# Kernel tuning notes

Measured on AMD Instinct MI355X. Metric: run time of the kernel, lower is better.

Reference implementation:

```python
import jax, jax.numpy as jnp
import numpy as np

VOCAB = 32000
EMBED = 512
DEP_SIZE = 64
QKV = 512
B, S = 16, 1024
NEG = -1e10


def setup_inputs() -> dict:
    key = jax.random.key(0)
    ks = jax.random.split(key, 16)
    inputs = jax.random.randint(ks[0], (B, S), 0, VOCAB)
    dependency = jax.random.randint(ks[1], (B, S, S), 0, DEP_SIZE)
    embed_table = jax.random.normal(ks[2], (VOCAB, EMBED), dtype=jnp.float32) * 0.02
    dep_table = jax.random.normal(ks[3], (DEP_SIZE, 1), dtype=jnp.float32) * 0.02
    dep_table = dep_table.at[0].set(0.0)  # padding_idx=0
    sc = 1.0 / np.sqrt(EMBED)
    Wq = jax.random.normal(ks[4], (EMBED, QKV), dtype=jnp.float32) * sc
    bq = jnp.zeros((QKV,), jnp.float32)
    Wk = jax.random.normal(ks[5], (EMBED, QKV), dtype=jnp.float32) * sc
    bk = jnp.zeros((QKV,), jnp.float32)
    Wv = jax.random.normal(ks[6], (EMBED, QKV), dtype=jnp.float32) * sc
    bv = jnp.zeros((QKV,), jnp.float32)
    scv = 1.0 / np.sqrt(QKV)
    W1 = jax.random.normal(ks[7], (QKV, QKV), dtype=jnp.float32) * scv
    b1 = jnp.zeros((QKV,), jnp.float32)
    W2 = jax.random.normal(ks[8], (QKV, QKV), dtype=jnp.float32) * scv
    b2 = jnp.zeros((QKV,), jnp.float32)
    return dict(inputs=inputs, dependency=dependency, embed_table=embed_table,
                dep_table=dep_table, Wq=Wq, bq=bq, Wk=Wk, bk=bk, Wv=Wv, bv=bv,
                W1=W1, b1=b1, W2=W2, b2=b2)


def reference(inputs, dependency, embed_table, dep_table, Wq, bq, Wk, bk, Wv, bv, W1, b1, W2, b2):
    x = jnp.take(embed_table, inputs, axis=0)                  # [B,S,E]
    dep_emb = jnp.take(dep_table, dependency, axis=0)[..., 0]  # [B,S,S]
    q = x @ Wq + bq                                            # [B,S,D]
    k = x @ Wk + bk
    v = x @ Wv + bv
    attn = jnp.einsum('bqd,bkd->bqk', q, k) * dep_emb          # [B,S,S]
    attn = jnp.where(dependency == 0, NEG, attn)
    weights = jax.nn.softmax(attn, axis=-1)
    wm = jnp.einsum('bqk,bkd->bqd', weights, v)                # fused weighted sum
    wm = jnp.tanh(wm @ W1 + b1) @ W2 + b2
    return wm, weights
```

## Files before the change

kernel.cpp:

```cpp
#include <hip/hip_runtime.h>

typedef __attribute__((ext_vector_type(8))) short short8;
typedef __attribute__((ext_vector_type(4))) float floatx4;

__device__ __forceinline__ unsigned short f2b(float f) {
  unsigned int u = __float_as_uint(f);
  unsigned int r = (u + 0x7FFFu + ((u >> 16) & 1u)) >> 16;
  return (unsigned short)r;
}
__device__ __forceinline__ uint4 ld8f(const float* p) {
  float4 a = *(const float4*)p;
  float4 b = *(const float4*)(p + 4);
  uint4 r;
  r.x = (unsigned int)f2b(a.x) | ((unsigned int)f2b(a.y) << 16);
  r.y = (unsigned int)f2b(a.z) | ((unsigned int)f2b(a.w) << 16);
  r.z = (unsigned int)f2b(b.x) | ((unsigned int)f2b(b.y) << 16);
  r.w = (unsigned int)f2b(b.z) | ((unsigned int)f2b(b.w) << 16);
  return r;
}

#define GLL(g, l) __builtin_amdgcn_global_load_lds( \
    (const __attribute__((address_space(1))) unsigned int*)(g), \
    (__attribute__((address_space(3))) unsigned int*)(l), 16, 0, 0)

__device__ __forceinline__ void xcd_swz(int& bx, int& by, int& bz) {
  const int nx = gridDim.x, ny = gridDim.y;
  const int nwg = nx * ny * gridDim.z;
  const int lbid = blockIdx.x + nx * (blockIdx.y + ny * blockIdx.z);
  const int s = (lbid & 7) * (nwg >> 3) + (lbid >> 3);
  bx = s % nx; by = (s / nx) % ny; bz = s / (nx * ny);
}

__device__ __forceinline__ void kloop(const unsigned short* __restrict__ A,
                                      const unsigned short* __restrict__ B,
                                      int K, unsigned short* ldsA, unsigned short* ldsB,
                                      floatx4 (&acc)[2][4])
{
  const int tid = threadIdx.x;
  const int w = tid >> 6, lane = tid & 63;
  const int quad = lane >> 4, l16 = lane & 15;
  const int wy = w >> 1, wx = w & 1;
  const int rsa = 16 * w + (lane >> 2);
  const int rsb = 32 * w + (lane >> 2);
  const int ks = (lane & 3) * 8;
  const int loa  = w * 512 + lane * 8;
  const int lob0 = w * 1024 + lane * 8;
  const int lob1 = lob0 + 512;
  const unsigned short* a0 = A + (size_t)rsa * K + ks;
  const unsigned short* b0 = B + (size_t)rsb * K + ks;
  const unsigned short* b1 = b0 + (size_t)16 * K;

  for (int k0 = 0; k0 < K; k0 += 32) {
    __syncthreads();
    GLL(a0 + k0, &ldsA[loa]);
    GLL(b0 + k0, &ldsB[lob0]);
    GLL(b1 + k0, &ldsB[lob1]);
    __syncthreads();
    short8 af[2], bf[4];
#pragma unroll
    for (int i = 0; i < 2; i++)
      af[i] = *(const short8*)&ldsA[(wy * 32 + i * 16 + l16) * 32 + quad * 8];
#pragma unroll
    for (int j = 0; j < 4; j++)
      bf[j] = *(const short8*)&ldsB[(wx * 64 + j * 16 + l16) * 32 + quad * 8];
#pragma unroll
    for (int i = 0; i < 2; i++)
#pragma unroll
      for (int j = 0; j < 4; j++)
        acc[i][j] = __builtin_amdgcn_mfma_f32_16x16x32_bf16(af[i], bf[j], acc[i][j], 0, 0, 0);
  }
}

__global__ __launch_bounds__(256, 4) void gemm_qkv(
    const unsigned short* __restrict__ x,
    const unsigned short* __restrict__ WT,
    const float* __restrict__ bq, const float* __restrict__ bk, const float* __restrict__ bv,
    unsigned short* __restrict__ q, unsigned short* __restrict__ kx, unsigned short* __restrict__ v)
{
  __shared__ unsigned short ldsA[2048], ldsB[4096];
  int bx, by, bz;
  xcd_swz(bx, by, bz);
  const int m0 = by * 64, n0 = bx * 128;
  floatx4 acc[2][4];
#pragma unroll
  for (int i = 0; i < 2; i++)
#pragma unroll
    for (int j = 0; j < 4; j++) acc[i][j] = (floatx4){0.f, 0.f, 0.f, 0.f};

  kloop(x + (size_t)m0 * 512, WT + (size_t)n0 * 512, 512, ldsA, ldsB, acc);

  const int seg = n0 >> 9, nloc = n0 & 511;
  unsigned short* C = seg == 0 ? q : (seg == 1 ? kx : v);
  const float* bias = seg == 0 ? bq : (seg == 1 ? bk : bv);
  const int lane = threadIdx.x & 63, w = threadIdx.x >> 6;
  const int quad = lane >> 4, l16 = lane & 15, wy = w >> 1, wx = w & 1;
  float bvv[4];
#pragma unroll
  for (int j = 0; j < 4; j++) bvv[j] = bias[nloc + wx * 64 + j * 16 + l16];
#pragma unroll
  for (int i = 0; i < 2; i++)
#pragma unroll
    for (int r = 0; r < 4; r++) {
      int m = m0 + wy * 32 + i * 16 + quad * 4 + r;
      unsigned short* crow = C + (size_t)m * 512 + nloc + wx * 64 + l16;
#pragma unroll
      for (int j = 0; j < 4; j++) crow[j * 16] = f2b(acc[i][j][r] + bvv[j]);
    }
}

template<int CF32, int ACT>
__global__ __launch_bounds__(256, 4) void gemm2(
    const unsigned short* __restrict__ A, const unsigned short* __restrict__ Bt,
    const float* __restrict__ bias, void* __restrict__ Cv,
    int N, int K, long aB, long bB, long cB)
{
  __shared__ unsigned short ldsA[2048], ldsB[4096];
  int bx, by, bz;
  xcd_swz(bx, by, bz);
  const int b = bz;
  const int m0 = by * 64, n0 = bx * 128;
  floatx4 acc[2][4];
#pragma unroll
  for (int i = 0; i < 2; i++)
#pragma unroll
    for (int j = 0; j < 4; j++) acc[i][j] = (floatx4){0.f, 0.f, 0.f, 0.f};

  kloop(A + (size_t)b * aB + (size_t)m0 * K, Bt + (size_t)b * bB + (size_t)n0 * K,
        K, ldsA, ldsB, acc);

  const int lane = threadIdx.x & 63, w = threadIdx.x >> 6;
  const int quad = lane >> 4, l16 = lane & 15, wy = w >> 1, wx = w & 1;
  float bvv[4];
#pragma unroll
  for (int j = 0; j < 4; j++)
    bvv[j] = bias ? bias[n0 + wx * 64 + j * 16 + l16] : 0.f;
  float*          Cf = (float*)Cv          + (size_t)b * cB;
  unsigned short* Ch = (unsigned short*)Cv + (size_t)b * cB;
#pragma unroll
  for (int i = 0; i < 2; i++)
#pragma unroll
    for (int r = 0; r < 4; r++) {
      int m = m0 + wy * 32 + i * 16 + quad * 4 + r;
      size_t base = (size_t)m * N + n0 + wx * 64 + l16;
#pragma unroll
      for (int j = 0; j < 4; j++) {
        float vv = acc[i][j][r] + bvv[j];
        if (ACT == 1) vv = tanhf(vv);
        if (CF32) Cf[base + j * 16] = vv;
        else      Ch[base + j * 16] = f2b(vv);
      }
    }
}

#define CST 132
__global__ __launch_bounds__(256, 4) void score_kernel(
    const unsigned short* __restrict__ Q, const unsigned short* __restrict__ Km,
    const int* __restrict__ dep, const float* __restrict__ dept,
    float* __restrict__ E)
{
  __shared__ union {
    struct { unsigned short a[2048]; unsigned short b[4096]; } s;
    float c[32 * CST];
  } sm;
  __shared__ float dtab[64];
  const int tid = threadIdx.x;
  if (tid < 64) dtab[tid] = dept[tid];

  int bx, by, bz;
  xcd_swz(bx, by, bz);
  const int b = bz;
  const int m0 = by * 64, n0 = bx * 128;
  floatx4 acc[2][4];
#pragma unroll
  for (int i = 0; i < 2; i++)
#pragma unroll
    for (int j = 0; j < 4; j++) acc[i][j] = (floatx4){0.f, 0.f, 0.f, 0.f};

  kloop(Q + (size_t)b * (1024 * 512) + (size_t)m0 * 512,
        Km + (size_t)b * (1024 * 512) + (size_t)n0 * 512,
        512, sm.s.a, sm.s.b, acc);

  const int lane = tid & 63, w = tid >> 6;
  const int quad = lane >> 4, l16 = lane & 15, wy = w >> 1, wx = w & 1;
  const int* depb = dep + (size_t)b * 1024 * 1024;
  float* Eb = E + (size_t)b * 1024 * 1024;
  const int cr = tid >> 3, cb = (tid & 7) * 16;

#pragma unroll
  for (int i = 0; i < 2; i++) {
    __syncthreads();
#pragma unroll
    for (int j = 0; j < 4; j++)
#pragma unroll
      for (int r = 0; r < 4; r++)
        sm.c[(wy * 16 + quad * 4 + r) * CST + wx * 64 + j * 16 + l16] = acc[i][j][r];
    __syncthreads();
    const int m = m0 + (cr >> 4) * 32 + i * 16 + (cr & 15);
    const int* dr = depb + (size_t)m * 1024 + n0 + cb;
    float* er = Eb + (size_t)m * 1024 + n0 + cb;
    const float* crow = &sm.c[cr * CST + cb];
#pragma unroll
    for (int c = 0; c < 4; c++) {
      int4 d = *(const int4*)(dr + c * 4);
      float4 s = *(const float4*)(crow + c * 4);
      float4 e;
      e.x = d.x ? __expf(fminf(fmaxf(s.x * dtab[d.x & 63], -60.f), 60.f)) : 0.f;
      e.y = d.y ? __expf(fminf(fmaxf(s.y * dtab[d.y & 63], -60.f), 60.f)) : 0.f;
      e.z = d.z ? __expf(fminf(fmaxf(s.z * dtab[d.z & 63], -60.f), 60.f)) : 0.f;
      e.w = d.w ? __expf(fminf(fmaxf(s.w * dtab[d.w & 63], -60.f), 60.f)) : 0.f;
      *(float4*)(er + c * 4) = e;
    }
  }
}

__global__ void build_x(const float* __restrict__ embed, const int* __restrict__ inputs,
                        unsigned short* __restrict__ x)
{
  const int row = blockIdx.x * 4 + (threadIdx.x >> 6);
  const int lane = threadIdx.x & 63;
  const float* src = embed + (size_t)inputs[row] * 512 + lane * 8;
  *(uint4*)&x[(size_t)row * 512 + lane * 8] = ld8f(src);
}

__global__ void trans_w(const float* s0, const float* s1, const float* s2,
                        const float* s3, const float* s4, unsigned short* dst)
{
  __shared__ unsigned short tile[32][33];
  const int z = blockIdx.z;
  const float* src = z == 0 ? s0 : z == 1 ? s1 : z == 2 ? s2 : z == 3 ? s3 : s4;
  unsigned short* ob = dst + (size_t)z * 262144;
  int c0 = blockIdx.x * 32, r0 = blockIdx.y * 32;
  int tx = threadIdx.x & 31, ty = threadIdx.x >> 5;
  for (int i = ty; i < 32; i += 8)
    tile[i][tx] = f2b(src[(size_t)(r0 + i) * 512 + (c0 + tx)]);
  __syncthreads();
  for (int i = ty; i < 32; i += 8)
    ob[(size_t)(c0 + i) * 512 + (r0 + tx)] = tile[tx][i];
}

__global__ void trans_v(const unsigned short* __restrict__ in, unsigned short* __restrict__ out)
{
  __shared__ unsigned short tile[32][33];
  const unsigned short* ib = in + (size_t)blockIdx.z * (1024 * 512);
  unsigned short* ob = out + (size_t)blockIdx.z * (512 * 1024);
  int c0 = blockIdx.x * 32, r0 = blockIdx.y * 32;
  int tx = threadIdx.x & 31, ty = threadIdx.x >> 5;
  for (int i = ty; i < 32; i += 8)
    tile[i][tx] = ib[(size_t)(r0 + i) * 512 + (c0 + tx)];
  __syncthreads();
  for (int i = ty; i < 32; i += 8)
    ob[(size_t)(c0 + i) * 1024 + (r0 + tx)] = tile[tx][i];
}

__global__ void normalize_rows(float* __restrict__ wf, unsigned short* __restrict__ wb)
{
  size_t row = blockIdx.x;
  float4* p = (float4*)(wf + row * 1024);
  float4 u = p[threadIdx.x];
  float s = (u.x + u.y) + (u.z + u.w);
#pragma unroll
  for (int d = 1; d < 64; d <<= 1) s += __shfl_xor(s, d);
  __shared__ float acc4[4];
  if ((threadIdx.x & 63) == 0) acc4[threadIdx.x >> 6] = s;
  __syncthreads();
  float tot = (acc4[0] + acc4[1]) + (acc4[2] + acc4[3]);
  float inv = tot > 0.f ? 1.f / tot : 0.f;
  u.x *= inv; u.y *= inv; u.z *= inv; u.w *= inv;
  p[threadIdx.x] = u;
  uint2 pk;
  pk.x = (unsigned int)f2b(u.x) | ((unsigned int)f2b(u.y) << 16);
  pk.y = (unsigned int)f2b(u.z) | ((unsigned int)f2b(u.w) << 16);
  *(uint2*)&wb[row * 1024 + threadIdx.x * 4] = pk;
}

extern "C" void kernel_launch(void* const* d_in, const int* in_sizes, int n_in,
                              void* d_out, int out_size, void* d_ws, size_t ws_size,
                              hipStream_t stream)
{
  const int*   inputs     = (const int*)d_in[0];
  const int*   dependency = (const int*)d_in[1];
  const float* embed      = (const float*)d_in[2];
  const float* dept       = (const float*)d_in[3];
  const float* Wq = (const float*)d_in[4];   const float* bq = (const float*)d_in[5];
  const float* Wk = (const float*)d_in[6];   const float* bk = (const float*)d_in[7];
  const float* Wv = (const float*)d_in[8];   const float* bvv = (const float*)d_in[9];
  const float* W1 = (const float*)d_in[10];  const float* b1 = (const float*)d_in[11];
  const float* W2 = (const float*)d_in[12];  const float* b2 = (const float*)d_in[13];

  float* out  = (float*)d_out;
  float* wout = out + (size_t)8388608;

  unsigned short* ws   = (unsigned short*)d_ws;
  unsigned short* q    = ws;
  unsigned short* kx   = ws + 8388608;
  unsigned short* WTc  = ws + 16777216;
  unsigned short* W1T  = ws + 17563648;
  unsigned short* W2T  = ws + 17825792;
  unsigned short* wbf  = ws;
  unsigned short* h    = ws;

  unsigned short* x    = (unsigned short*)wout;
  unsigned short* v    = (unsigned short*)out;
  unsigned short* vT   = (unsigned short*)out + 8388608;
  unsigned short* wmp  = (unsigned short*)out;

  dim3 blk(256);

  trans_w<<<dim3(16, 16, 5), blk, 0, stream>>>(Wq, Wk, Wv, W1, W2, WTc);
  build_x<<<dim3(4096), blk, 0, stream>>>(embed, inputs, x);

  gemm_qkv<<<dim3(12, 256, 1), blk, 0, stream>>>(x, WTc, bq, bk, bvv, q, kx, v);

  score_kernel<<<dim3(8, 16, 16), blk, 0, stream>>>(q, kx, dependency, dept, wout);

  trans_v<<<dim3(16, 32, 16), blk, 0, stream>>>(v, vT);

  normalize_rows<<<dim3(16384), blk, 0, stream>>>(wout, wbf);

  gemm2<0, 0><<<dim3(4, 16, 16), blk, 0, stream>>>(wbf, vT, nullptr, wmp,
                                                   512, 1024, 1024L * 1024, 512L * 1024, 1024L * 512);
  gemm2<0, 1><<<dim3(4, 256, 1), blk, 0, stream>>>(wmp, W1T, b1, h, 512, 512, 0, 0, 0);
  gemm2<1, 0><<<dim3(4, 256, 1), blk, 0, stream>>>(h, W2T, b2, out, 512, 512, 0, 0, 0);
}
```

Baseline: 400.2 us.

## Add 4-stage LDS prefetch pipeline and XOR swizzle to shared GEMM k-loop

Replaces the single-buffered k-loop (sync, load, sync, compute) with a four-slot ring buffer that issues global-to-LDS loads three tiles ahead and waits with explicit vmcnt counts, so memory latency overlaps MFMA work. Adds an XOR swizzle on the k-chunk index for both writes and reads to reduce LDS bank conflicts. LDS per block grows fourfold, and launch bounds drop to 3 blocks per CU, lowering occupancy. The score kernel's epilogue union also grows with the larger staging arrays.

```diff
diff --git a/kernel.cpp b/kernel.cpp
--- a/kernel.cpp
+++ b/kernel.cpp
@@ -42,42 +42,65 @@
   const int wy = w >> 1, wx = w & 1;
   const int rsa = 16 * w + (lane >> 2);
   const int rsb = 32 * w + (lane >> 2);
-  const int ks = (lane & 3) * 8;
+  const int ks = ((lane & 3) ^ ((lane >> 3) & 3)) * 8;
   const int loa  = w * 512 + lane * 8;
   const int lob0 = w * 1024 + lane * 8;
   const int lob1 = lob0 + 512;
+  const int sw = (l16 >> 1) & 3;
   const unsigned short* a0 = A + (size_t)rsa * K + ks;
   const unsigned short* b0 = B + (size_t)rsb * K + ks;
   const unsigned short* b1 = b0 + (size_t)16 * K;
-
-  for (int k0 = 0; k0 < K; k0 += 32) {
-    __syncthreads();
-    GLL(a0 + k0, &ldsA[loa]);
-    GLL(b0 + k0, &ldsB[lob0]);
-    GLL(b1 + k0, &ldsB[lob1]);
-    __syncthreads();
+  const int NT = K >> 5;
+
+#pragma unroll
+  for (int t = 0; t < 3; ++t) {
+    GLL(a0 + t * 32, &ldsA[t * 2048 + loa]);
+    GLL(b0 + t * 32, &ldsB[t * 4096 + lob0]);
+    GLL(b1 + t * 32, &ldsB[t * 4096 + lob1]);
+  }
+
+  for (int t = 0; t < NT; ++t) {
+    if (t + 3 < NT) {
+      const int s = (t + 3) & 3;
+      const int k0 = (t + 3) * 32;
+      GLL(a0 + k0, &ldsA[s * 2048 + loa]);
+      GLL(b0 + k0, &ldsB[s * 4096 + lob0]);
+      GLL(b1 + k0, &ldsB[s * 4096 + lob1]);
+      asm volatile("s_waitcnt vmcnt(9)" ::: "memory");
+    } else if (t + 3 == NT) {
+      asm volatile("s_waitcnt vmcnt(6)" ::: "memory");
+    } else if (t + 2 == NT) {
+      asm volatile("s_waitcnt vmcnt(3)" ::: "memory");
+    } else {
+      asm volatile("s_waitcnt vmcnt(0)" ::: "memory");
+    }
+    __builtin_amdgcn_s_barrier();
+    asm volatile("" ::: "memory");
+    const int c = t & 3;
     short8 af[2], bf[4];
 #pragma unroll
     for (int i = 0; i < 2; i++)
-      af[i] = *(const short8*)&ldsA[(wy * 32 + i * 16 + l16) * 32 + quad * 8];
+      af[i] = *(const short8*)&ldsA[c * 2048 + (wy * 32 + i * 16 + l16) * 32 + (quad ^ sw) * 8];
 #pragma unroll
     for (int j = 0; j < 4; j++)
-      bf[j] = *(const short8*)&ldsB[(wx * 64 + j * 16 + l16) * 32 + quad * 8];
+      bf[j] = *(const short8*)&ldsB[c * 4096 + (wx * 64 + j * 16 + l16) * 32 + (quad ^ sw) * 8];
 #pragma unroll
     for (int i = 0; i < 2; i++)
 #pragma unroll
       for (int j = 0; j < 4; j++)
         acc[i][j] = __builtin_amdgcn_mfma_f32_16x16x32_bf16(af[i], bf[j], acc[i][j], 0, 0, 0);
+    __builtin_amdgcn_s_barrier();
+    asm volatile("" ::: "memory");
   }
 }
 
-__global__ __launch_bounds__(256, 4) void gemm_qkv(
+__global__ __launch_bounds__(256, 3) void gemm_qkv(
     const unsigned short* __restrict__ x,
     const unsigned short* __restrict__ WT,
     const float* __restrict__ bq, const float* __restrict__ bk, const float* __restrict__ bv,
     unsigned short* __restrict__ q, unsigned short* __restrict__ kx, unsigned short* __restrict__ v)
 {
-  __shared__ unsigned short ldsA[2048], ldsB[4096];
+  __shared__ unsigned short ldsA[8192], ldsB[16384];
   int bx, by, bz;
   xcd_swz(bx, by, bz);
   const int m0 = by * 64, n0 = bx * 128;
@@ -109,12 +132,12 @@
 }
 
 template<int CF32, int ACT>
-__global__ __launch_bounds__(256, 4) void gemm2(
+__global__ __launch_bounds__(256, 3) void gemm2(
     const unsigned short* __restrict__ A, const unsigned short* __restrict__ Bt,
     const float* __restrict__ bias, void* __restrict__ Cv,
     int N, int K, long aB, long bB, long cB)
 {
-  __shared__ unsigned short ldsA[2048], ldsB[4096];
+  __shared__ unsigned short ldsA[8192], ldsB[16384];
   int bx, by, bz;
   xcd_swz(bx, by, bz);
   const int b = bz;
@@ -153,13 +176,13 @@
 }
 
 #define CST 132
-__global__ __launch_bounds__(256, 4) void score_kernel(
+__global__ __launch_bounds__(256, 3) void score_kernel(
     const unsigned short* __restrict__ Q, const unsigned short* __restrict__ Km,
     const int* __restrict__ dep, const float* __restrict__ dept,
     float* __restrict__ E)
 {
   __shared__ union {
-    struct { unsigned short a[2048]; unsigned short b[4096]; } s;
+    struct { unsigned short a[8192]; unsigned short b[16384]; } s;
     float c[32 * CST];
   } sm;
   __shared__ float dtab[64];
```

New measurement: 417.6 us. 4.4% more time.

## Double-buffer GEMM k-loop with register-staged prefetch instead of direct LDS loads

Applied to the files above, without the earlier changes.

Replaces the global_load_lds path in the shared k-loop with a register-staged software pipeline. The next K tile is loaded into registers while MFMAs run on the current LDS buffer, then written into the alternate LDS buffer, leaving one barrier per iteration instead of two. This is meant to hide global-load latency behind the matrix work. In exchange it doubles LDS per block, adds register pressure, and lowers launch_bounds occupancy from 4 to 3.

```diff
diff --git a/kernel.cpp b/kernel.cpp
--- a/kernel.cpp
+++ b/kernel.cpp
@@ -18,10 +18,6 @@
   r.w = (unsigned int)f2b(b.z) | ((unsigned int)f2b(b.w) << 16);
   return r;
 }
-
-#define GLL(g, l) __builtin_amdgcn_global_load_lds( \
-    (const __attribute__((address_space(1))) unsigned int*)(g), \
-    (__attribute__((address_space(3))) unsigned int*)(l), 16, 0, 0)
 
 __device__ __forceinline__ void xcd_swz(int& bx, int& by, int& bz) {
   const int nx = gridDim.x, ny = gridDim.y;
@@ -46,38 +42,62 @@
   const int loa  = w * 512 + lane * 8;
   const int lob0 = w * 1024 + lane * 8;
   const int lob1 = lob0 + 512;
-  const unsigned short* a0 = A + (size_t)rsa * K + ks;
-  const unsigned short* b0 = B + (size_t)rsb * K + ks;
-  const unsigned short* b1 = b0 + (size_t)16 * K;
-
-  for (int k0 = 0; k0 < K; k0 += 32) {
-    __syncthreads();
-    GLL(a0 + k0, &ldsA[loa]);
-    GLL(b0 + k0, &ldsB[lob0]);
-    GLL(b1 + k0, &ldsB[lob1]);
-    __syncthreads();
+  const unsigned short* ga  = A + (size_t)rsa * K + ks;
+  const unsigned short* gb0 = B + (size_t)rsb * K + ks;
+  const unsigned short* gb1 = gb0 + (size_t)16 * K;
+  const int NT = K >> 5;
+
+  uint4 va  = *(const uint4*)ga;
+  uint4 vb0 = *(const uint4*)gb0;
+  uint4 vb1 = *(const uint4*)gb1;
+  *(uint4*)&ldsA[loa]  = va;
+  *(uint4*)&ldsB[lob0] = vb0;
+  *(uint4*)&ldsB[lob1] = vb1;
+  asm volatile("s_waitcnt lgkmcnt(0)" ::: "memory");
+  __builtin_amdgcn_s_barrier();
+  __builtin_amdgcn_sched_barrier(0);
+
+  int p = 0;
+  for (int t = 0; t < NT; ++t) {
+    if (t + 1 < NT) {
+      const int k0 = (t + 1) * 32;
+      va  = *(const uint4*)(ga + k0);
+      vb0 = *(const uint4*)(gb0 + k0);
+      vb1 = *(const uint4*)(gb1 + k0);
+    }
+    const int cb = p ? 2048 : 0, cbB = p ? 4096 : 0;
     short8 af[2], bf[4];
 #pragma unroll
     for (int i = 0; i < 2; i++)
-      af[i] = *(const short8*)&ldsA[(wy * 32 + i * 16 + l16) * 32 + quad * 8];
+      af[i] = *(const short8*)&ldsA[cb + (wy * 32 + i * 16 + l16) * 32 + quad * 8];
 #pragma unroll
     for (int j = 0; j < 4; j++)
-      bf[j] = *(const short8*)&ldsB[(wx * 64 + j * 16 + l16) * 32 + quad * 8];
+      bf[j] = *(const short8*)&ldsB[cbB + (wx * 64 + j * 16 + l16) * 32 + quad * 8];
 #pragma unroll
     for (int i = 0; i < 2; i++)
 #pragma unroll
       for (int j = 0; j < 4; j++)
         acc[i][j] = __builtin_amdgcn_mfma_f32_16x16x32_bf16(af[i], bf[j], acc[i][j], 0, 0, 0);
+    if (t + 1 < NT) {
+      const int nb = p ? 0 : 2048, nbB = p ? 0 : 4096;
+      *(uint4*)&ldsA[nb + loa]   = va;
+      *(uint4*)&ldsB[nbB + lob0] = vb0;
+      *(uint4*)&ldsB[nbB + lob1] = vb1;
+    }
+    asm volatile("s_waitcnt lgkmcnt(0)" ::: "memory");
+    __builtin_amdgcn_s_barrier();
+    __builtin_amdgcn_sched_barrier(0);
+    p ^= 1;
   }
 }
 
-__global__ __launch_bounds__(256, 4) void gemm_qkv(
+__global__ __launch_bounds__(256, 3) void gemm_qkv(
     const unsigned short* __restrict__ x,
     const unsigned short* __restrict__ WT,
     const float* __restrict__ bq, const float* __restrict__ bk, const float* __restrict__ bv,
     unsigned short* __restrict__ q, unsigned short* __restrict__ kx, unsigned short* __restrict__ v)
 {
-  __shared__ unsigned short ldsA[2048], ldsB[4096];
+  __shared__ unsigned short ldsA[4096], ldsB[8192];
   int bx, by, bz;
   xcd_swz(bx, by, bz);
   const int m0 = by * 64, n0 = bx * 128;
@@ -109,12 +129,12 @@
 }
 
 template<int CF32, int ACT>
-__global__ __launch_bounds__(256, 4) void gemm2(
+__global__ __launch_bounds__(256, 3) void gemm2(
     const unsigned short* __restrict__ A, const unsigned short* __restrict__ Bt,
     const float* __restrict__ bias, void* __restrict__ Cv,
     int N, int K, long aB, long bB, long cB)
 {
-  __shared__ unsigned short ldsA[2048], ldsB[4096];
+  __shared__ unsigned short ldsA[4096], ldsB[8192];
   int bx, by, bz;
   xcd_swz(bx, by, bz);
   const int b = bz;
@@ -153,13 +173,13 @@
 }
 
 #define CST 132
-__global__ __launch_bounds__(256, 4) void score_kernel(
+__global__ __launch_bounds__(256, 3) void score_kernel(
     const unsigned short* __restrict__ Q, const unsigned short* __restrict__ Km,
     const int* __restrict__ dep, const float* __restrict__ dept,
     float* __restrict__ E)
 {
   __shared__ union {
-    struct { unsigned short a[2048]; unsigned short b[4096]; } s;
+    struct { unsigned short a[4096]; unsigned short b[8192]; } s;
     float c[32 * CST];
   } sm;
   __shared__ float dtab[64];
```

New measurement: 397.2 us. About the same (-0.7%).

## Switch all GEMMs to double-buffered 256x256 tiles with 512-thread blocks

Applied to the files above, without the earlier changes.

Replaces the 64x128 single-buffered k-loop with a 256x256 tile per 512-thread block, where each wave computes a 128x64 sub-tile. The next K-slice is prefetched into a second LDS buffer with explicit vmcnt waits, raw barriers and setprio around the MFMA burst. The score kernel drops its LDS staging of scores and writes straight from accumulators, reading the dep table from global memory. Larger tiles cut redundant global loads and barrier overhead, at the cost of far fewer blocks (e.g. 256 for scores, 128 for the W1/W2 GEMMs) and uncoalesced scattered stores in the epilogue.

```diff
diff --git a/kernel.cpp b/kernel.cpp
--- a/kernel.cpp
+++ b/kernel.cpp
@@ -31,117 +31,129 @@
   bx = s % nx; by = (s / nx) % ny; bz = s / (nx * ny);
 }
 
-__device__ __forceinline__ void kloop(const unsigned short* __restrict__ A,
-                                      const unsigned short* __restrict__ B,
-                                      int K, unsigned short* ldsA, unsigned short* ldsB,
-                                      floatx4 (&acc)[2][4])
+__device__ __forceinline__ void kloop256(const unsigned short* __restrict__ A,
+                                         const unsigned short* __restrict__ B,
+                                         int K, unsigned short* ldsA, unsigned short* ldsB,
+                                         floatx4 (&acc)[8][4])
 {
   const int tid = threadIdx.x;
   const int w = tid >> 6, lane = tid & 63;
   const int quad = lane >> 4, l16 = lane & 15;
-  const int wy = w >> 1, wx = w & 1;
-  const int rsa = 16 * w + (lane >> 2);
-  const int rsb = 32 * w + (lane >> 2);
-  const int ks = (lane & 3) * 8;
-  const int loa  = w * 512 + lane * 8;
-  const int lob0 = w * 1024 + lane * 8;
-  const int lob1 = lob0 + 512;
-  const unsigned short* a0 = A + (size_t)rsa * K + ks;
-  const unsigned short* b0 = B + (size_t)rsb * K + ks;
-  const unsigned short* b1 = b0 + (size_t)16 * K;
-
-  for (int k0 = 0; k0 < K; k0 += 32) {
-    __syncthreads();
-    GLL(a0 + k0, &ldsA[loa]);
-    GLL(b0 + k0, &ldsB[lob0]);
-    GLL(b1 + k0, &ldsB[lob1]);
-    __syncthreads();
-    short8 af[2], bf[4];
-#pragma unroll
-    for (int i = 0; i < 2; i++)
-      af[i] = *(const short8*)&ldsA[(wy * 32 + i * 16 + l16) * 32 + quad * 8];
+  const int wr = w >> 2, wc = w & 3;
+  const int srow = tid >> 2;
+  const int ks = (tid & 3) * 8;
+  const int ldst = tid * 8;
+  const unsigned short* gA0 = A + (size_t)srow * K + ks;
+  const unsigned short* gA1 = gA0 + (size_t)128 * K;
+  const unsigned short* gB0 = B + (size_t)srow * K + ks;
+  const unsigned short* gB1 = gB0 + (size_t)128 * K;
+  const int NT = K >> 5;
+
+  GLL(gA0, &ldsA[ldst]);
+  GLL(gA1, &ldsA[4096 + ldst]);
+  GLL(gB0, &ldsB[ldst]);
+  GLL(gB1, &ldsB[4096 + ldst]);
+
+  int cur = 0;
+  for (int t = 0; t < NT; ++t) {
+    const int nb = cur ^ 8192;
+    if (t + 1 < NT) {
+      const int k0 = (t + 1) * 32;
+      GLL(gA0 + k0, &ldsA[nb + ldst]);
+      GLL(gA1 + k0, &ldsA[nb + 4096 + ldst]);
+      GLL(gB0 + k0, &ldsB[nb + ldst]);
+      GLL(gB1 + k0, &ldsB[nb + 4096 + ldst]);
+      asm volatile("s_waitcnt vmcnt(4)" ::: "memory");
+    } else {
+      asm volatile("s_waitcnt vmcnt(0)" ::: "memory");
+    }
+    __builtin_amdgcn_s_barrier();
+    __builtin_amdgcn_sched_barrier(0);
+    short8 af[8], bf[4];
+#pragma unroll
+    for (int i = 0; i < 8; i++)
+      af[i] = *(const short8*)&ldsA[cur + (wr * 128 + i * 16 + l16) * 32 + quad * 8];
 #pragma unroll
     for (int j = 0; j < 4; j++)
-      bf[j] = *(const short8*)&ldsB[(wx * 64 + j * 16 + l16) * 32 + quad * 8];
-#pragma unroll
-    for (int i = 0; i < 2; i++)
+      bf[j] = *(const short8*)&ldsB[cur + (wc * 64 + j * 16 + l16) * 32 + quad * 8];
+    __builtin_amdgcn_s_setprio(1);
+#pragma unroll
+    for (int i = 0; i < 8; i++)
 #pragma unroll
       for (int j = 0; j < 4; j++)
         acc[i][j] = __builtin_amdgcn_mfma_f32_16x16x32_bf16(af[i], bf[j], acc[i][j], 0, 0, 0);
+    __builtin_amdgcn_s_setprio(0);
+    __builtin_amdgcn_s_barrier();
+    __builtin_amdgcn_sched_barrier(0);
+    cur = nb;
   }
 }
 
-__global__ __launch_bounds__(256, 4) void gemm_qkv(
+#define ACC_INIT floatx4 acc[8][4]; \
+  _Pragma("unroll") for (int i = 0; i < 8; i++) \
+  _Pragma("unroll") for (int j = 0; j < 4; j++) acc[i][j] = (floatx4){0.f, 0.f, 0.f, 0.f};
+
+__global__ __launch_bounds__(512, 2) void gemm_qkv(
     const unsigned short* __restrict__ x,
     const unsigned short* __restrict__ WT,
     const float* __restrict__ bq, const float* __restrict__ bk, const float* __restrict__ bv,
     unsigned short* __restrict__ q, unsigned short* __restrict__ kx, unsigned short* __restrict__ v)
 {
-  __shared__ unsigned short ldsA[2048], ldsB[4096];
+  __shared__ unsigned short ldsA[16384], ldsB[16384];
   int bx, by, bz;
   xcd_swz(bx, by, bz);
-  const int m0 = by * 64, n0 = bx * 128;
-  floatx4 acc[2][4];
-#pragma unroll
-  for (int i = 0; i < 2; i++)
-#pragma unroll
-    for (int j = 0; j < 4; j++) acc[i][j] = (floatx4){0.f, 0.f, 0.f, 0.f};
-
-  kloop(x + (size_t)m0 * 512, WT + (size_t)n0 * 512, 512, ldsA, ldsB, acc);
+  const int m0 = by * 256, n0 = bx * 256;
+  ACC_INIT
+  kloop256(x + (size_t)m0 * 512, WT + (size_t)n0 * 512, 512, ldsA, ldsB, acc);
 
   const int seg = n0 >> 9, nloc = n0 & 511;
   unsigned short* C = seg == 0 ? q : (seg == 1 ? kx : v);
   const float* bias = seg == 0 ? bq : (seg == 1 ? bk : bv);
   const int lane = threadIdx.x & 63, w = threadIdx.x >> 6;
-  const int quad = lane >> 4, l16 = lane & 15, wy = w >> 1, wx = w & 1;
+  const int quad = lane >> 4, l16 = lane & 15, wr = w >> 2, wc = w & 3;
   float bvv[4];
 #pragma unroll
-  for (int j = 0; j < 4; j++) bvv[j] = bias[nloc + wx * 64 + j * 16 + l16];
-#pragma unroll
-  for (int i = 0; i < 2; i++)
+  for (int j = 0; j < 4; j++) bvv[j] = bias[nloc + wc * 64 + j * 16 + l16];
+#pragma unroll
+  for (int i = 0; i < 8; i++)
 #pragma unroll
     for (int r = 0; r < 4; r++) {
-      int m = m0 + wy * 32 + i * 16 + quad * 4 + r;
-      unsigned short* crow = C + (size_t)m * 512 + nloc + wx * 64 + l16;
+      int m = m0 + wr * 128 + i * 16 + quad * 4 + r;
+      unsigned short* crow = C + (size_t)m * 512 + nloc + wc * 64 + l16;
 #pragma unroll
       for (int j = 0; j < 4; j++) crow[j * 16] = f2b(acc[i][j][r] + bvv[j]);
     }
 }
 
 template<int CF32, int ACT>
-__global__ __launch_bounds__(256, 4) void gemm2(
+__global__ __launch_bounds__(512, 2) void gemm2(
     const unsigned short* __restrict__ A, const unsigned short* __restrict__ Bt,
     const float* __restrict__ bias, void* __restrict__ Cv,
     int N, int K, long aB, long bB, long cB)
 {
-  __shared__ unsigned short ldsA[2048], ldsB[4096];
+  __shared__ unsigned short ldsA[16384], ldsB[16384];
   int bx, by, bz;
   xcd_swz(bx, by, bz);
   const int b = bz;
-  const int m0 = by * 64, n0 = bx * 128;
-  floatx4 acc[2][4];
-#pragma unroll
-  for (int i = 0; i < 2; i++)
-#pragma unroll
-    for (int j = 0; j < 4; j++) acc[i][j] = (floatx4){0.f, 0.f, 0.f, 0.f};
-
-  kloop(A + (size_t)b * aB + (size_t)m0 * K, Bt + (size_t)b * bB + (size_t)n0 * K,
-        K, ldsA, ldsB, acc);
+  const int m0 = by * 256, n0 = bx * 256;
+  ACC_INIT
+  kloop256(A + (size_t)b * aB + (size_t)m0 * K, Bt + (size_t)b * bB + (size_t)n0 * K,
+           K, ldsA, ldsB, acc);
 
   const int lane = threadIdx.x & 63, w = threadIdx.x >> 6;
-  const int quad = lane >> 4, l16 = lane & 15, wy = w >> 1, wx = w & 1;
+  const int quad = lane >> 4, l16 = lane & 15, wr = w >> 2, wc = w & 3;
   float bvv[4];
 #pragma unroll
   for (int j = 0; j < 4; j++)
-    bvv[j] = bias ? bias[n0 + wx * 64 + j * 16 + l16] : 0.f;
+    bvv[j] = bias ? bias[n0 + wc * 64 + j * 16 + l16] : 0.f;
   float*          Cf = (float*)Cv          + (size_t)b * cB;
   unsigned short* Ch = (unsigned short*)Cv + (size_t)b * cB;
 #pragma unroll
-  for (int i = 0; i < 2; i++)
+  for (int i = 0; i < 8; i++)
 #pragma unroll
     for (int r = 0; r < 4; r++) {
-      int m = m0 + wy * 32 + i * 16 + quad * 4 + r;
-      size_t base = (size_t)m * N + n0 + wx * 64 + l16;
+      int m = m0 + wr * 128 + i * 16 + quad * 4 + r;
+      size_t base = (size_t)m * N + n0 + wc * 64 + l16;
 #pragma unroll
       for (int j = 0; j < 4; j++) {
         float vv = acc[i][j][r] + bvv[j];
@@ -152,65 +164,40 @@
     }
 }
 
-#define CST 132
-__global__ __launch_bounds__(256, 4) void score_kernel(
+__global__ __launch_bounds__(512, 2) void score_kernel(
     const unsigned short* __restrict__ Q, const unsigned short* __restrict__ Km,
     const int* __restrict__ dep, const float* __restrict__ dept,
     float* __restrict__ E)
 {
-  __shared__ union {
-    struct { unsigned short a[2048]; unsigned short b[4096]; } s;
-    float c[32 * CST];
-  } sm;
-  __shared__ float dtab[64];
-  const int tid = threadIdx.x;
-  if (tid < 64) dtab[tid] = dept[tid];
-
+  __shared__ unsigned short ldsA[16384], ldsB[16384];
   int bx, by, bz;
   xcd_swz(bx, by, bz);
   const int b = bz;
-  const int m0 = by * 64, n0 = bx * 128;
-  floatx4 acc[2][4];
-#pragma unroll
-  for (int i = 0; i < 2; i++)
-#pragma unroll
-    for (int j = 0; j < 4; j++) acc[i][j] = (floatx4){0.f, 0.f, 0.f, 0.f};
-
-  kloop(Q + (size_t)b * (1024 * 512) + (size_t)m0 * 512,
-        Km + (size_t)b * (1024 * 512) + (size_t)n0 * 512,
-        512, sm.s.a, sm.s.b, acc);
-
+  const int m0 = by * 256, n0 = bx * 256;
+  ACC_INIT
+  kloop256(Q + (size_t)b * (1024 * 512) + (size_t)m0 * 512,
+           Km + (size_t)b * (1024 * 512) + (size_t)n0 * 512,
+           512, ldsA, ldsB, acc);
+
+  const int tid = threadIdx.x;
   const int lane = tid & 63, w = tid >> 6;
-  const int quad = lane >> 4, l16 = lane & 15, wy = w >> 1, wx = w & 1;
+  const int quad = lane >> 4, l16 = lane & 15, wr = w >> 2, wc = w & 3;
   const int* depb = dep + (size_t)b * 1024 * 1024;
   float* Eb = E + (size_t)b * 1024 * 1024;
-  const int cr = tid >> 3, cb = (tid & 7) * 16;
-
-#pragma unroll
-  for (int i = 0; i < 2; i++) {
-    __syncthreads();
-#pragma unroll
-    for (int j = 0; j < 4; j++)
-#pragma unroll
-      for (int r = 0; r < 4; r++)
-        sm.c[(wy * 16 + quad * 4 + r) * CST + wx * 64 + j * 16 + l16] = acc[i][j][r];
-    __syncthreads();
-    const int m = m0 + (cr >> 4) * 32 + i * 16 + (cr & 15);
-    const int* dr = depb + (size_t)m * 1024 + n0 + cb;
-    float* er = Eb + (size_t)m * 1024 + n0 + cb;
-    const float* crow = &sm.c[cr * CST + cb];
-#pragma unroll
-    for (int c = 0; c < 4; c++) {
-      int4 d = *(const int4*)(dr + c * 4);
-      float4 s = *(const float4*)(crow + c * 4);
-      float4 e;
-      e.x = d.x ? __expf(fminf(fmaxf(s.x * dtab[d.x & 63], -60.f), 60.f)) : 0.f;
-      e.y = d.y ? __expf(fminf(fmaxf(s.y * dtab[d.y & 63], -60.f), 60.f)) : 0.f;
-      e.z = d.z ? __expf(fminf(fmaxf(s.z * dtab[d.z & 63], -60.f), 60.f)) : 0.f;
-      e.w = d.w ? __expf(fminf(fmaxf(s.w * dtab[d.w & 63], -60.f), 60.f)) : 0.f;
-      *(float4*)(er + c * 4) = e;
+#pragma unroll
+  for (int i = 0; i < 8; i++)
+#pragma unroll
+    for (int r = 0; r < 4; r++) {
+      const int m = m0 + wr * 128 + i * 16 + quad * 4 + r;
+      const int* dr = depb + (size_t)m * 1024 + n0 + wc * 64 + l16;
+      float* er = Eb + (size_t)m * 1024 + n0 + wc * 64 + l16;
+#pragma unroll
+      for (int j = 0; j < 4; j++) {
+        int d = dr[j * 16];
+        float s = acc[i][j][r];
+        er[j * 16] = d ? __expf(fminf(fmaxf(s * dept[d & 63], -60.f), 60.f)) : 0.f;
+      }
     }
-  }
 }
 
 __global__ void build_x(const float* __restrict__ embed, const int* __restrict__ inputs,
@@ -304,21 +291,21 @@
   unsigned short* vT   = (unsigned short*)out + 8388608;
   unsigned short* wmp  = (unsigned short*)out;
 
-  dim3 blk(256);
+  dim3 blk(256), blk5(512);
 
   trans_w<<<dim3(16, 16, 5), blk, 0, stream>>>(Wq, Wk, Wv, W1, W2, WTc);
   build_x<<<dim3(4096), blk, 0, stream>>>(embed, inputs, x);
 
-  gemm_qkv<<<dim3(12, 256, 1), blk, 0, stream>>>(x, WTc, bq, bk, bvv, q, kx, v);
-
-  score_kernel<<<dim3(8, 16, 16), blk, 0, stream>>>(q, kx, dependency, dept, wout);
+  gemm_qkv<<<dim3(6, 64, 1), blk5, 0, stream>>>(x, WTc, bq, bk, bvv, q, kx, v);
+
+  score_kernel<<<dim3(4, 4, 16), blk5, 0, stream>>>(q, kx, dependency, dept, wout);
 
   trans_v<<<dim3(16, 32, 16), blk, 0, stream>>>(v, vT);
 
   normalize_rows<<<dim3(16384), blk, 0, stream>>>(wout, wbf);
 
-  gemm2<0, 0><<<dim3(4, 16, 16), blk, 0, stream>>>(wbf, vT, nullptr, wmp,
+  gemm2<0, 0><<<dim3(2, 4, 16), blk5, 0, stream>>>(wbf, vT, nullptr, wmp,
                                                    512, 1024, 1024L * 1024, 512L * 1024, 1024L * 512);
-  gemm2<0, 1><<<dim3(4, 256, 1), blk, 0, stream>>>(wmp, W1T, b1, h, 512, 512, 0, 0, 0);
-  gemm2<1, 0><<<dim3(4, 256, 1), blk, 0, stream>>>(h, W2T, b2, out, 512, 512, 0, 0, 0);
-}
+  gemm2<0, 1><<<dim3(2, 64, 1), blk5, 0, stream>>>(wmp, W1T, b1, h, 512, 512, 0, 0, 0);
+  gemm2<1, 0><<<dim3(2, 64, 1), blk5, 0, stream>>>(h, W2T, b2, out, 512, 512, 0, 0, 0);
+}
```

Result: slower. 502.5 us (+25.6%).
